# Kernel optimization log

Hardware: AMD Instinct MI355X
Metric: run time of the kernel (lower is better)

The kernel has to match this reference:

```python
import jax, jax.numpy as jnp
import numpy as np
from jax import lax

B, S, D, T = 64, 256, 1024, 60
HIST = 20  # last-20 window of attn / decoder-state history


def setup_inputs() -> dict:
    key = jax.random.key(0)
    ks = jax.random.split(key, 8)
    e_outputs = jax.random.normal(ks[0], (B, S, D), jnp.float32)
    queries = jax.random.normal(ks[1], (B, T, D), jnp.float32)
    # attention weights over source frames: rows sum to 1
    attns = jax.nn.softmax(jax.random.normal(ks[2], (B, T, S), jnp.float32), axis=-1)
    g = 0.02
    Wr = jax.random.normal(ks[3], (D, 1), jnp.float32) * g
    br = jnp.zeros((1,), jnp.float32)
    Wa = jax.random.normal(ks[4], (D, 1), jnp.float32) * g
    ba = jnp.zeros((1,), jnp.float32)
    Wq = jax.random.normal(ks[5], (D, D), jnp.float32) / np.sqrt(D)
    Wn = jax.random.normal(ks[6], (2 * D, 1), jnp.float32) * g
    bn = jnp.zeros((1,), jnp.float32)
    return {"e_outputs": e_outputs, "queries": queries, "attns": attns,
            "Wr": Wr, "br": br, "Wa": Wa, "ba": ba, "Wq": Wq, "Wn": Wn, "bn": bn}


def reference(e_outputs, queries, attns, Wr, br, Wa, ba, Wq, Wn, bn):
    Bn, Sn, Dn = e_outputs.shape
    # decay1[i] = (i+1)/20 ; decay2[i] = 1-(i+1)/50, zero-padded past 50 frames
    decay1 = (jnp.arange(HIST, dtype=jnp.float32) + 1.0) / 20.0
    idx = jnp.arange(Sn, dtype=jnp.float32)
    add0 = jnp.where(idx < 50, 1.0 - (idx + 1.0) / 50.0, 0.0)
    add_state0 = add0[None, :, None]                       # [1,S,1]
    mem0 = e_outputs * add_state0                          # [B,S,D]
    abuf0 = jnp.zeros((HIST, Bn, Sn), e_outputs.dtype)
    qbuf0 = jnp.zeros((HIST, Bn, Dn), e_outputs.dtype)

    def step(carry, x):
        mem, add_state, abuf, qbuf, i = carry
        attn_i, q_i = x                                    # [B,S], [B,D]
        # read: selected frame before memory update
        sel = jnp.einsum('bs,bsd->bd', attn_i, mem)
        # roll history buffers (newest at slot HIST-1)
        abuf = jnp.concatenate([abuf[1:], attn_i[None]], axis=0)
        qbuf = jnp.concatenate([qbuf[1:], q_i[None]], axis=0)
        k = jnp.minimum(i + 1, HIST)
        valid = jnp.arange(HIST) >= (HIST - k)
        temp = jax.nn.softmax(jnp.where(valid, decay1, -jnp.inf))
        attn_w = jnp.einsum('t,tbs->bs', temp, abuf)       # decayed attn sum
        query_s = jnp.einsum('t,tbd->bd', temp, qbuf)      # decayed query sum
        remove_prob = jax.nn.sigmoid(q_i @ Wr + br)[:, :, None]   # [B,1,1]
        add_prob = jax.nn.sigmoid(q_i @ Wa + ba)[:, :, None]      # [B,1,1]
        sim = jax.nn.sigmoid(jnp.einsum('bsd,bd->bs', mem, query_s @ Wq))[..., None]
        mem = mem * (1.0 - remove_prob * attn_w[..., None] * sim)
        last_ctx = jnp.einsum('bs,bsd->bd', attn_w, e_outputs)[:, None, :]
        cat = jnp.concatenate([e_outputs, jnp.broadcast_to(last_ctx, e_outputs.shape)], axis=-1)
        nxt = jax.nn.sigmoid(cat @ Wn + bn)                # [B,S,1]
        mem = mem + e_outputs * (1.0 - add_state) * (add_prob * nxt)
        add_state = add_state + (1.0 - add_state) * (add_prob * nxt)
        return (mem, add_state, abuf, qbuf, i + 1), sel

    init = (mem0, jnp.broadcast_to(add_state0, (Bn, Sn, 1)), abuf0, qbuf0, jnp.int32(0))
    xs = (attns.transpose(1, 0, 2), queries.transpose(1, 0, 2))
    _, sels = lax.scan(step, init, xs)
    return sels.transpose(1, 0, 2)                         # [B,T,D]
```

## Files before the change

### kernel.cpp

```cpp
#include <hip/hip_runtime.h>
#include <math.h>


#define Bn 64
#define Sn 256
#define Dn 1024
#define Tn 60
#define HISTn 20
#define LDK 72
#define K05 1.0512710963760241f
#define EINV 0.36787944117144233f

typedef __bf16 bf16x8 __attribute__((ext_vector_type(8)));
typedef float f32x4 __attribute__((ext_vector_type(4)));
typedef unsigned short us8 __attribute__((ext_vector_type(8)));

typedef const __attribute__((address_space(1))) unsigned int* gas_u32p;
typedef __attribute__((address_space(3))) unsigned int* las_u32p;

__device__ __forceinline__ void gl16(const unsigned short* g, unsigned short* l){
  __builtin_amdgcn_global_load_lds((gas_u32p)g, (las_u32p)l, 16, 0, 0);
}

__device__ __forceinline__ unsigned short f2bf(float f){
  unsigned int x; __builtin_memcpy(&x,&f,4);
  unsigned int lsb = (x >> 16) & 1u;
  x += 0x7fffu + lsb;
  return (unsigned short)(x >> 16);
}
__device__ __forceinline__ float sigmoidf_(float x){ return 1.0f/(1.0f+expf(-x)); }

__global__ __launch_bounds__(256) void conv_fused(
    const float* __restrict__ Q, const float* __restrict__ Wr,
    const float* __restrict__ br, const float* __restrict__ Wa,
    const float* __restrict__ ba, const float* __restrict__ Wq,
    const float* __restrict__ E, const float* __restrict__ Wn,
    float* __restrict__ rp, float* __restrict__ ap,
    unsigned short* __restrict__ Qbf, unsigned short* __restrict__ WT,
    unsigned short* __restrict__ Ebf,
    float* __restrict__ eW1, float* __restrict__ eW2)
{
  int tid = threadIdx.x;
  int bx = blockIdx.x;
  if (bx < Bn*Tn){
    int row = bx;
    float4 x = ((const float4*)(Q + (size_t)row*Dn))[tid];
    float4 a = ((const float4*)Wr)[tid];
    float4 b = ((const float4*)Wa)[tid];
    unsigned short o[4] = {f2bf(x.x), f2bf(x.y), f2bf(x.z), f2bf(x.w)};
    *(uint2*)&Qbf[(size_t)row*Dn + tid*4] = *(uint2*)o;
    float s1 = x.x*a.x + x.y*a.y + x.z*a.z + x.w*a.w;
    float s2 = x.x*b.x + x.y*b.y + x.z*b.z + x.w*b.w;
    for (int off = 32; off; off >>= 1){
      s1 += __shfl_down(s1, off, 64);
      s2 += __shfl_down(s2, off, 64);
    }
    __shared__ float r1[4], r2[4];
    int lane = tid & 63, wv = tid >> 6;
    if (lane == 0){ r1[wv] = s1; r2[wv] = s2; }
    __syncthreads();
    if (tid == 0){
      rp[row] = sigmoidf_(r1[0]+r1[1]+r1[2]+r1[3] + br[0]);
      ap[row] = sigmoidf_(r2[0]+r2[1]+r2[2]+r2[3] + ba[0]);
    }
  } else if (bx < Bn*Tn + 256){
    __shared__ __align__(16) unsigned short Tt[64][LDK];
    int t = bx - Bn*Tn;
    int n0 = (t >> 4)*64, k0 = (t & 15)*64;
    int kl = tid >> 4, nl4 = (tid & 15)*4;
    #pragma unroll
    for (int it = 0; it < 4; it++){
      int k = kl + it*16;
      float4 v = *(const float4*)&Wq[(size_t)(k0+k)*Dn + n0 + nl4];
      Tt[nl4+0][k] = f2bf(v.x); Tt[nl4+1][k] = f2bf(v.y);
      Tt[nl4+2][k] = f2bf(v.z); Tt[nl4+3][k] = f2bf(v.w);
    }
    __syncthreads();
    int nr = tid >> 2, kg = (tid & 3)*16;
    *(us8*)&WT[(size_t)(n0+nr)*Dn + k0+kg]   = *(us8*)&Tt[nr][kg];
    *(us8*)&WT[(size_t)(n0+nr)*Dn + k0+kg+8] = *(us8*)&Tt[nr][kg+8];
  } else {
    int row = (bx - (Bn*Tn + 256))*4 + (tid >> 6);
    int lane = tid & 63;
    const float* er = E + (size_t)row*Dn;
    unsigned short* ebr = Ebf + (size_t)row*Dn;
    float d1 = 0.f, d2 = 0.f;
    #pragma unroll
    for (int c = 0; c < 4; c++){
      int idx = c*64 + lane;
      float4 v = ((const float4*)er)[idx];
      float4 w1 = ((const float4*)Wn)[idx];
      float4 w2 = ((const float4*)(Wn + Dn))[idx];
      unsigned short o[4] = {f2bf(v.x), f2bf(v.y), f2bf(v.z), f2bf(v.w)};
      ((uint2*)ebr)[idx] = *(uint2*)o;
      d1 += v.x*w1.x + v.y*w1.y + v.z*w1.z + v.w*w1.w;
      d2 += v.x*w2.x + v.y*w2.y + v.z*w2.z + v.w*w2.w;
    }
    #pragma unroll
    for (int off = 32; off; off >>= 1){
      d1 += __shfl_down(d1, off, 64);
      d2 += __shfl_down(d2, off, 64);
    }
    if (lane == 0){ eW1[row] = d1; eW2[row] = d2; }
  }
}

__global__ __launch_bounds__(256) void gemm_qw_kr(
    const unsigned short* __restrict__ Qbf,
    const unsigned short* __restrict__ WT,
    const float* __restrict__ At,
    const float* __restrict__ eW2,
    unsigned short* __restrict__ QWbf,
    float* __restrict__ lc)
{
  int tid = threadIdx.x;
  if (blockIdx.x < (Bn*Tn/64)*(Dn/64)){
    __shared__ __align__(16) unsigned short As0_[64*64], Bs0_[64*64];
    __shared__ __align__(16) unsigned short As1_[64*64], Bs1_[64*64];
    int bx = (blockIdx.x & 7)*120 + (blockIdx.x >> 3);
    int m0 = (bx >> 4) * 64, n0 = (bx & 15) * 64;
    int lane = tid & 63, wave = tid >> 6;
    int quad = lane >> 4, l16 = lane & 15;
    f32x4 acc[4];
    #pragma unroll
    for (int nt=0;nt<4;nt++)
      #pragma unroll
      for (int r=0;r<4;r++) acc[nt][r]=0.f;
    int c0 = wave*2;
    int srow = c0*8 + (lane >> 3);
    int scol = ((lane & 7) ^ (lane >> 3)) * 8;
    const unsigned short* gA0 = Qbf + (size_t)(m0 + srow)*Dn + scol;
    const unsigned short* gA1 = gA0 + 8*Dn;
    const unsigned short* gB0 = WT  + (size_t)(n0 + srow)*Dn + scol;
    const unsigned short* gB1 = gB0 + 8*Dn;
    int mrow = wave*16 + l16;

    #define STAGE_QW(K, A_, B_) { \
      gl16(gA0 + (K), &A_[c0*512]);       \
      gl16(gA1 + (K), &A_[c0*512 + 512]); \
      gl16(gB0 + (K), &B_[c0*512]);       \
      gl16(gB1 + (K), &B_[c0*512 + 512]); }
    #define COMP_QW(A_, B_) { \
      _Pragma("unroll") \
      for (int kk = 0; kk < 2; kk++){ \
        bf16x8 a = *(const bf16x8*)&A_[ mrow*64 + ((kk*32 + quad*8) ^ ((mrow&7)*8)) ]; \
        _Pragma("unroll") \
        for (int nt=0;nt<4;nt++){ \
          int nrow = nt*16 + l16; \
          bf16x8 bb = *(const bf16x8*)&B_[ nrow*64 + ((kk*32 + quad*8) ^ ((nrow&7)*8)) ]; \
          acc[nt] = __builtin_amdgcn_mfma_f32_16x16x32_bf16(a, bb, acc[nt], 0, 0, 0); \
        } \
      } }

    STAGE_QW(0, As0_, Bs0_);
    __syncthreads();
    #pragma unroll
    for (int k0 = 0; k0 < Dn; k0 += 128){
      STAGE_QW(k0+64, As1_, Bs1_);
      COMP_QW(As0_, Bs0_);
      __syncthreads();
      if (k0+128 < Dn) STAGE_QW(k0+128, As0_, Bs0_);
      COMP_QW(As1_, Bs1_);
      __syncthreads();
    }
    #undef STAGE_QW
    #undef COMP_QW

    #pragma unroll
    for (int nt=0;nt<4;nt++)
      #pragma unroll
      for (int r=0;r<4;r++){
        int m = m0 + wave*16 + quad*4 + r;
        int n = n0 + nt*16 + l16;
        QWbf[(size_t)m*Dn + n] = f2bf(acc[nt][r]);
      }
  } else {
    int b = blockIdx.x - (Bn*Tn/64)*(Dn/64);
    int lane = tid & 63, wv = tid >> 6;
    __shared__ float Rsh[Tn];
    float4 e2v = ((const float4*)(eW2 + (size_t)b*Sn))[lane];
    const float* at_b = At + (size_t)b*Tn*Sn;
    #pragma unroll
    for (int w = 0; w < 15; w++){
      int j = wv + w*4;
      float4 a4 = ((const float4*)(at_b + (size_t)j*Sn))[lane];
      float v = a4.x*e2v.x + a4.y*e2v.y + a4.z*e2v.z + a4.w*e2v.w;
      #pragma unroll
      for (int off = 32; off; off >>= 1) v += __shfl_down(v, off, 64);
      if (lane == 0) Rsh[j] = v;
    }
    __syncthreads();
    if (tid < Tn){
      int i = tid;
      int j0 = (i - HISTn + 1 > 0) ? i - HISTn + 1 : 0;
      float num = 0.f, den = 0.f;
      float wj = 1.f;
      for (int j = 0; j <= i; j++){
        wj *= K05;
        if (j >= j0){ num += wj * Rsh[j]; den += wj; }
      }
      lc[b*Tn + i] = num / den;
    }
  }
}

__global__ __launch_bounds__(256) void g_scan(
    const unsigned short* __restrict__ QWbf,
    const unsigned short* __restrict__ Ebf,
    const float* __restrict__ At,
    const float* __restrict__ rp,
    const float* __restrict__ ap,
    const float* __restrict__ eW1,
    const float* __restrict__ lc,
    const float* __restrict__ bnp,
    unsigned short* __restrict__ Pbf)
{
  __shared__ __align__(16) unsigned short As0_[64][LDK], Bs0_[64][LDK];
  __shared__ __align__(16) unsigned short As1_[64][LDK], Bs1_[64][LDK];
  __shared__ __align__(16) float AtL[Tn][64], GL[Tn][64];
  __shared__ float lcs[Tn], rps[Tn], aps[Tn];
  int b = blockIdx.x, s0 = blockIdx.y * 64;
  int tid = threadIdx.x, lane = tid & 63, wave = tid >> 6;
  int quad = lane >> 4, l16 = lane & 15;

  const float* at_b = At + (size_t)b*Tn*Sn + s0;
  #pragma unroll
  for (int it = 0; it < 4; it++){
    int r = it*16 + (tid >> 4);
    if (r < Tn){
      int c4 = (tid & 15)*4;
      *(float4*)&AtL[r][c4] = *(const float4*)&at_b[(size_t)r*Sn + c4];
    }
  }
  if (tid < Tn){
    lcs[tid] = lc[b*Tn + tid];
    rps[tid] = rp[b*Tn + tid];
    aps[tid] = ap[b*Tn + tid];
  }

  f32x4 acc[4];
  #pragma unroll
  for (int nt=0;nt<4;nt++)
    #pragma unroll
    for (int r=0;r<4;r++) acc[nt][r]=0.f;
  int sr = tid >> 2, sk = (tid & 3)*16;
  const unsigned short* aRow = QWbf + ((size_t)(b*Tn + sr))*Dn;
  const unsigned short* bRow = Ebf  + ((size_t)(b*Sn + s0 + sr))*Dn;

  #define LOADR(K, ra0, ra1, rb0, rb1) { \
    if (sr < Tn){ ra0 = *(const us8*)&aRow[(K)+sk]; ra1 = *(const us8*)&aRow[(K)+sk+8]; } \
    else { ra0 = (us8)0; ra1 = (us8)0; } \
    rb0 = *(const us8*)&bRow[(K)+sk]; rb1 = *(const us8*)&bRow[(K)+sk+8]; }
  #define STORER(A_, B_, ra0, ra1, rb0, rb1) { \
    *(us8*)&A_[sr][sk]   = ra0; *(us8*)&A_[sr][sk+8] = ra1; \
    *(us8*)&B_[sr][sk]   = rb0; *(us8*)&B_[sr][sk+8] = rb1; }
  #define COMP_G(A_, B_) { \
    _Pragma("unroll") \
    for (int kk = 0; kk < 64; kk += 32){ \
      bf16x8 a = *(const bf16x8*)&A_[wave*16 + l16][kk + quad*8]; \
      _Pragma("unroll") \
      for (int nt=0;nt<4;nt++){ \
        bf16x8 bb = *(const bf16x8*)&B_[nt*16 + l16][kk + quad*8]; \
        acc[nt] = __builtin_amdgcn_mfma_f32_16x16x32_bf16(a, bb, acc[nt], 0, 0, 0); \
      } \
    } }

  us8 pa0, pa1, pb0, pb1, qa0, qa1, qb0, qb1;
  LOADR(0, pa0, pa1, pb0, pb1);
  STORER(As0_, Bs0_, pa0, pa1, pb0, pb1);
  for (int k0 = 0; k0 < Dn; k0 += 128){
    LOADR(k0+64, qa0, qa1, qb0, qb1);
    __syncthreads();
    COMP_G(As0_, Bs0_);
    STORER(As1_, Bs1_, qa0, qa1, qb0, qb1);
    if (k0+128 < Dn) LOADR(k0+128, pa0, pa1, pb0, pb1);
    __syncthreads();
    COMP_G(As1_, Bs1_);
    if (k0+128 < Dn) STORER(As0_, Bs0_, pa0, pa1, pb0, pb1);
  }
  #undef LOADR
  #undef STORER
  #undef COMP_G

  #pragma unroll
  for (int nt=0;nt<4;nt++)
    #pragma unroll
    for (int r=0;r<4;r++){
      int t = wave*16 + quad*4 + r;
      if (t < Tn) GL[t][nt*16 + l16] = acc[nt][r];
    }
  __syncthreads();

  if (tid < 64){
    int s = s0 + tid;
    float M = (s < 50) ? (1.0f - (s+1)/50.0f) : 0.0f;
    float A = M;
    float bnv = bnp[0];
    float e1 = eW1[b*Sn + s];
    unsigned short* P_b = Pbf + (size_t)b*Tn*Sn + s;
    float num_a = 0.f, num_q = 0.f, den = 0.f, wi = 1.f;
    #pragma unroll
    for (int i = 0; i < Tn; i++){
      wi *= K05;
      float a_new = AtL[i][tid];
      float g_new = GL[i][tid];
      num_a += wi * a_new;
      num_q += wi * g_new;
      den   += wi;
      if (i >= HISTn){
        float wo = wi * EINV;
        num_a -= wo * AtL[i-HISTn][tid];
        num_q -= wo * GL[i-HISTn][tid];
        den   -= wo;
      }
      float inv = 1.0f / den;
      float aw = num_a * inv;
      float qd = num_q * inv;
      P_b[(size_t)i*Sn] = f2bf(a_new * M);
      float sim = sigmoidf_(M * qd);
      float nxt = sigmoidf_(e1 + lcs[i] + bnv);
      M = M * (1.0f - rps[i] * aw * sim);
      float g = (1.0f - A) * aps[i] * nxt;
      M += g; A += g;
    }
  }
}

__global__ __launch_bounds__(256) void gemm_sels(
    const unsigned short* __restrict__ Pbf,
    const unsigned short* __restrict__ Ebf,
    float* __restrict__ out)
{
  __shared__ __align__(16) unsigned short As0_[64][LDK], Bs0_[64][LDK];
  __shared__ __align__(16) unsigned short As1_[64][LDK], Bs1_[64][LDK];
  int b = blockIdx.x, n0 = blockIdx.y*64;
  int tid = threadIdx.x, lane = tid & 63, wave = tid >> 6;
  int quad = lane >> 4, l16 = lane & 15;
  f32x4 acc[4];
  #pragma unroll
  for (int nt=0;nt<4;nt++)
    #pragma unroll
    for (int r=0;r<4;r++) acc[nt][r]=0.f;
  int sr = tid >> 2, sk = (tid & 3)*16;

  #define SLOAD(K, ra0, ra1, re0, re1) { \
    if (sr < Tn){ \
      const unsigned short* pp = &Pbf[((size_t)(b*Tn + sr))*Sn + (K)+sk]; \
      ra0 = *(const us8*)pp; ra1 = *(const us8*)(pp+8); \
    } else { ra0 = (us8)0; ra1 = (us8)0; } \
    const unsigned short* ep = &Ebf[((size_t)(b*Sn + (K) + sr))*Dn + n0 + sk]; \
    re0 = *(const us8*)ep; re1 = *(const us8*)(ep + 8); }
  #define SSTORE(A_, B_, ra0, ra1, re0, re1) { \
    *(us8*)&A_[sr][sk]   = ra0; *(us8*)&A_[sr][sk+8] = ra1; \
    _Pragma("unroll") \
    for (int j=0;j<8;j++){ \
      B_[sk+j][sr]   = re0[j]; \
      B_[sk+8+j][sr] = re1[j]; } }
  #define COMP_S(A_, B_) { \
    _Pragma("unroll") \
    for (int kk = 0; kk < 64; kk += 32){ \
      bf16x8 a = *(const bf16x8*)&A_[wave*16 + l16][kk + quad*8]; \
      _Pragma("unroll") \
      for (int nt=0;nt<4;nt++){ \
        bf16x8 bb = *(const bf16x8*)&B_[nt*16 + l16][kk + quad*8]; \
        acc[nt] = __builtin_amdgcn_mfma_f32_16x16x32_bf16(a, bb, acc[nt], 0, 0, 0); \
      } \
    } }

  us8 pa0, pa1, pe0, pe1, qa0, qa1, qe0, qe1;
  SLOAD(0, pa0, pa1, pe0, pe1);
  SSTORE(As0_, Bs0_, pa0, pa1, pe0, pe1);
  #pragma unroll
  for (int k0 = 0; k0 < Sn; k0 += 128){
    SLOAD(k0+64, qa0, qa1, qe0, qe1);
    __syncthreads();
    COMP_S(As0_, Bs0_);
    SSTORE(As1_, Bs1_, qa0, qa1, qe0, qe1);
    if (k0+128 < Sn) SLOAD(k0+128, pa0, pa1, pe0, pe1);
    __syncthreads();
    COMP_S(As1_, Bs1_);
    if (k0+128 < Sn) SSTORE(As0_, Bs0_, pa0, pa1, pe0, pe1);
  }
  #undef SLOAD
  #undef SSTORE
  #undef COMP_S

  #pragma unroll
  for (int nt=0;nt<4;nt++)
    #pragma unroll
    for (int r=0;r<4;r++){
      int t = wave*16 + quad*4 + r;
      int d = n0 + nt*16 + l16;
      if (t < Tn) out[((size_t)(b*Tn + t))*Dn + d] = acc[nt][r];
    }
}

extern "C" void kernel_launch(void* const* d_in, const int* in_sizes, int n_in,
                              void* d_out, int out_size, void* d_ws, size_t ws_size,
                              hipStream_t stream)
{
  const float* E  = (const float*)d_in[0];
  const float* Q  = (const float*)d_in[1];
  const float* At = (const float*)d_in[2];
  const float* Wr = (const float*)d_in[3];
  const float* br = (const float*)d_in[4];
  const float* Wa = (const float*)d_in[5];
  const float* ba = (const float*)d_in[6];
  const float* Wq = (const float*)d_in[7];
  const float* Wn = (const float*)d_in[8];
  const float* bnp= (const float*)d_in[9];

  char* ws = (char*)d_ws;
  float* rp  = (float*)ws; ws += (size_t)Bn*Tn*4;
  float* ap  = (float*)ws; ws += (size_t)Bn*Tn*4;
  float* eW1 = (float*)ws; ws += (size_t)Bn*Sn*4;
  float* eW2 = (float*)ws; ws += (size_t)Bn*Sn*4;
  float* lcb = (float*)ws; ws += (size_t)Bn*Tn*4;
  unsigned short* Qbf  = (unsigned short*)ws; ws += (size_t)Bn*Tn*Dn*2;
  unsigned short* WT   = (unsigned short*)ws; ws += (size_t)Dn*Dn*2;
  unsigned short* QWbf = (unsigned short*)ws; ws += (size_t)Bn*Tn*Dn*2;
  unsigned short* Ebf  = (unsigned short*)ws; ws += (size_t)Bn*Sn*Dn*2;
  unsigned short* Pbf = (unsigned short*)ws; ws += (size_t)Bn*Tn*Sn*2;

  conv_fused<<<Bn*Tn + 256 + Bn*Sn/4, 256, 0, stream>>>(
      Q, Wr, br, Wa, ba, Wq, E, Wn, rp, ap, Qbf, WT, Ebf, eW1, eW2);
  gemm_qw_kr<<<(Bn*Tn/64)*(Dn/64) + Bn, 256, 0, stream>>>(
      Qbf, WT, At, eW2, QWbf, lcb);
  g_scan<<<dim3(Bn, Sn/64), 256, 0, stream>>>(
      QWbf, Ebf, At, rp, ap, eW1, lcb, bnp, Pbf);
  gemm_sels<<<dim3(Bn, Dn/64), 256, 0, stream>>>(Pbf, Ebf, (float*)d_out);
}
```

Baseline: 184.1 us.

## Rebalance kernel stages: move E conversion into QW GEMM, fuse lc into scan

The E fp32-to-bf16 conversion and Wn dot products move from the first kernel into the QW GEMM launch as extra blocks. The per-batch lc computation (attn·eW2 plus a decayed window sum) moves into g_scan, where each block recomputes it redundantly. g_scan now uses 32-column S tiles, which doubles its grid, and gemm_sels drops from a double-buffered LDS pipeline to a single buffer. The aim is to even out work across launches and give the scan stage more parallelism, at the cost of redundant lc work per block and less load/compute overlap in gemm_sels.

```diff
diff --git a/kernel.cpp b/kernel.cpp
--- a/kernel.cpp
+++ b/kernel.cpp
@@ -30,15 +30,12 @@
 }
 __device__ __forceinline__ float sigmoidf_(float x){ return 1.0f/(1.0f+expf(-x)); }
 
-__global__ __launch_bounds__(256) void conv_fused(
+__global__ __launch_bounds__(256) void convQW(
     const float* __restrict__ Q, const float* __restrict__ Wr,
     const float* __restrict__ br, const float* __restrict__ Wa,
     const float* __restrict__ ba, const float* __restrict__ Wq,
-    const float* __restrict__ E, const float* __restrict__ Wn,
     float* __restrict__ rp, float* __restrict__ ap,
-    unsigned short* __restrict__ Qbf, unsigned short* __restrict__ WT,
-    unsigned short* __restrict__ Ebf,
-    float* __restrict__ eW1, float* __restrict__ eW2)
+    unsigned short* __restrict__ Qbf, unsigned short* __restrict__ WT)
 {
   int tid = threadIdx.x;
   int bx = blockIdx.x;
@@ -63,7 +60,7 @@
       rp[row] = sigmoidf_(r1[0]+r1[1]+r1[2]+r1[3] + br[0]);
       ap[row] = sigmoidf_(r2[0]+r2[1]+r2[2]+r2[3] + ba[0]);
     }
-  } else if (bx < Bn*Tn + 256){
+  } else {
     __shared__ __align__(16) unsigned short Tt[64][LDK];
     int t = bx - Bn*Tn;
     int n0 = (t >> 4)*64, k0 = (t & 15)*64;
@@ -79,39 +76,16 @@
     int nr = tid >> 2, kg = (tid & 3)*16;
     *(us8*)&WT[(size_t)(n0+nr)*Dn + k0+kg]   = *(us8*)&Tt[nr][kg];
     *(us8*)&WT[(size_t)(n0+nr)*Dn + k0+kg+8] = *(us8*)&Tt[nr][kg+8];
-  } else {
-    int row = (bx - (Bn*Tn + 256))*4 + (tid >> 6);
-    int lane = tid & 63;
-    const float* er = E + (size_t)row*Dn;
-    unsigned short* ebr = Ebf + (size_t)row*Dn;
-    float d1 = 0.f, d2 = 0.f;
-    #pragma unroll
-    for (int c = 0; c < 4; c++){
-      int idx = c*64 + lane;
-      float4 v = ((const float4*)er)[idx];
-      float4 w1 = ((const float4*)Wn)[idx];
-      float4 w2 = ((const float4*)(Wn + Dn))[idx];
-      unsigned short o[4] = {f2bf(v.x), f2bf(v.y), f2bf(v.z), f2bf(v.w)};
-      ((uint2*)ebr)[idx] = *(uint2*)o;
-      d1 += v.x*w1.x + v.y*w1.y + v.z*w1.z + v.w*w1.w;
-      d2 += v.x*w2.x + v.y*w2.y + v.z*w2.z + v.w*w2.w;
-    }
-    #pragma unroll
-    for (int off = 32; off; off >>= 1){
-      d1 += __shfl_down(d1, off, 64);
-      d2 += __shfl_down(d2, off, 64);
-    }
-    if (lane == 0){ eW1[row] = d1; eW2[row] = d2; }
-  }
-}
-
-__global__ __launch_bounds__(256) void gemm_qw_kr(
+  }
+}
+
+__global__ __launch_bounds__(256) void qw_e(
     const unsigned short* __restrict__ Qbf,
     const unsigned short* __restrict__ WT,
-    const float* __restrict__ At,
-    const float* __restrict__ eW2,
+    const float* __restrict__ E, const float* __restrict__ Wn,
     unsigned short* __restrict__ QWbf,
-    float* __restrict__ lc)
+    unsigned short* __restrict__ Ebf,
+    float* __restrict__ eW1, float* __restrict__ eW2)
 {
   int tid = threadIdx.x;
   if (blockIdx.x < (Bn*Tn/64)*(Dn/64)){
@@ -175,32 +149,28 @@
         QWbf[(size_t)m*Dn + n] = f2bf(acc[nt][r]);
       }
   } else {
-    int b = blockIdx.x - (Bn*Tn/64)*(Dn/64);
-    int lane = tid & 63, wv = tid >> 6;
-    __shared__ float Rsh[Tn];
-    float4 e2v = ((const float4*)(eW2 + (size_t)b*Sn))[lane];
-    const float* at_b = At + (size_t)b*Tn*Sn;
-    #pragma unroll
-    for (int w = 0; w < 15; w++){
-      int j = wv + w*4;
-      float4 a4 = ((const float4*)(at_b + (size_t)j*Sn))[lane];
-      float v = a4.x*e2v.x + a4.y*e2v.y + a4.z*e2v.z + a4.w*e2v.w;
-      #pragma unroll
-      for (int off = 32; off; off >>= 1) v += __shfl_down(v, off, 64);
-      if (lane == 0) Rsh[j] = v;
-    }
-    __syncthreads();
-    if (tid < Tn){
-      int i = tid;
-      int j0 = (i - HISTn + 1 > 0) ? i - HISTn + 1 : 0;
-      float num = 0.f, den = 0.f;
-      float wj = 1.f;
-      for (int j = 0; j <= i; j++){
-        wj *= K05;
-        if (j >= j0){ num += wj * Rsh[j]; den += wj; }
-      }
-      lc[b*Tn + i] = num / den;
-    }
+    int row = (blockIdx.x - (Bn*Tn/64)*(Dn/64))*4 + (tid >> 6);
+    int lane = tid & 63;
+    const float* er = E + (size_t)row*Dn;
+    unsigned short* ebr = Ebf + (size_t)row*Dn;
+    float d1 = 0.f, d2 = 0.f;
+    #pragma unroll
+    for (int c = 0; c < 4; c++){
+      int idx = c*64 + lane;
+      float4 v = ((const float4*)er)[idx];
+      float4 w1 = ((const float4*)Wn)[idx];
+      float4 w2 = ((const float4*)(Wn + Dn))[idx];
+      unsigned short o[4] = {f2bf(v.x), f2bf(v.y), f2bf(v.z), f2bf(v.w)};
+      ((uint2*)ebr)[idx] = *(uint2*)o;
+      d1 += v.x*w1.x + v.y*w1.y + v.z*w1.z + v.w*w1.w;
+      d2 += v.x*w2.x + v.y*w2.y + v.z*w2.z + v.w*w2.w;
+    }
+    #pragma unroll
+    for (int off = 32; off; off >>= 1){
+      d1 += __shfl_down(d1, off, 64);
+      d2 += __shfl_down(d2, off, 64);
+    }
+    if (lane == 0){ eW1[row] = d1; eW2[row] = d2; }
   }
 }
 
@@ -211,79 +181,92 @@
     const float* __restrict__ rp,
     const float* __restrict__ ap,
     const float* __restrict__ eW1,
-    const float* __restrict__ lc,
+    const float* __restrict__ eW2,
     const float* __restrict__ bnp,
     unsigned short* __restrict__ Pbf)
 {
-  __shared__ __align__(16) unsigned short As0_[64][LDK], Bs0_[64][LDK];
-  __shared__ __align__(16) unsigned short As1_[64][LDK], Bs1_[64][LDK];
-  __shared__ __align__(16) float AtL[Tn][64], GL[Tn][64];
-  __shared__ float lcs[Tn], rps[Tn], aps[Tn];
-  int b = blockIdx.x, s0 = blockIdx.y * 64;
+  __shared__ __align__(16) unsigned short As0_[64][LDK], As1_[64][LDK];
+  __shared__ __align__(16) unsigned short Bs0_[32][LDK], Bs1_[32][LDK];
+  __shared__ __align__(16) float AtL[Tn][32], GL[Tn][32];
+  __shared__ float Rsh[Tn], lcs[Tn], rps[Tn], aps[Tn];
+  int b = blockIdx.x, s0 = blockIdx.y * 32;
   int tid = threadIdx.x, lane = tid & 63, wave = tid >> 6;
   int quad = lane >> 4, l16 = lane & 15;
 
-  const float* at_b = At + (size_t)b*Tn*Sn + s0;
-  #pragma unroll
-  for (int it = 0; it < 4; it++){
-    int r = it*16 + (tid >> 4);
-    if (r < Tn){
-      int c4 = (tid & 15)*4;
-      *(float4*)&AtL[r][c4] = *(const float4*)&at_b[(size_t)r*Sn + c4];
+  {
+    float4 e2v = ((const float4*)(eW2 + (size_t)b*Sn))[lane];
+    const float* at_b = At + (size_t)b*Tn*Sn;
+    #pragma unroll
+    for (int w = 0; w < 15; w++){
+      int j = wave + w*4;
+      float4 a4 = ((const float4*)(at_b + (size_t)j*Sn))[lane];
+      float v = a4.x*e2v.x + a4.y*e2v.y + a4.z*e2v.z + a4.w*e2v.w;
+      #pragma unroll
+      for (int off = 32; off; off >>= 1) v += __shfl_down(v, off, 64);
+      if (lane == 0) Rsh[j] = v;
+    }
+  }
+  {
+    const float* at_c = At + (size_t)b*Tn*Sn + s0;
+    #pragma unroll
+    for (int it = 0; it < 2; it++){
+      int idx = it*256 + tid;
+      int r = idx >> 3, c4 = (idx & 7)*4;
+      if (r < Tn) *(float4*)&AtL[r][c4] = *(const float4*)&at_c[(size_t)r*Sn + c4];
     }
   }
   if (tid < Tn){
-    lcs[tid] = lc[b*Tn + tid];
     rps[tid] = rp[b*Tn + tid];
     aps[tid] = ap[b*Tn + tid];
   }
 
-  f32x4 acc[4];
+  f32x4 acc[2];
   #pragma unroll
-  for (int nt=0;nt<4;nt++)
+  for (int nt=0;nt<2;nt++)
     #pragma unroll
     for (int r=0;r<4;r++) acc[nt][r]=0.f;
   int sr = tid >> 2, sk = (tid & 3)*16;
+  int brw = tid >> 3, bk = (tid & 7)*8;
   const unsigned short* aRow = QWbf + ((size_t)(b*Tn + sr))*Dn;
-  const unsigned short* bRow = Ebf  + ((size_t)(b*Sn + s0 + sr))*Dn;
-
-  #define LOADR(K, ra0, ra1, rb0, rb1) { \
+  const unsigned short* bRow = Ebf  + ((size_t)(b*Sn + s0 + brw))*Dn;
+
+  #define LOADR(K, ra0, ra1, rb0) { \
     if (sr < Tn){ ra0 = *(const us8*)&aRow[(K)+sk]; ra1 = *(const us8*)&aRow[(K)+sk+8]; } \
     else { ra0 = (us8)0; ra1 = (us8)0; } \
-    rb0 = *(const us8*)&bRow[(K)+sk]; rb1 = *(const us8*)&bRow[(K)+sk+8]; }
-  #define STORER(A_, B_, ra0, ra1, rb0, rb1) { \
+    rb0 = *(const us8*)&bRow[(K)+bk]; }
+  #define STORER(A_, B_, ra0, ra1, rb0) { \
     *(us8*)&A_[sr][sk]   = ra0; *(us8*)&A_[sr][sk+8] = ra1; \
-    *(us8*)&B_[sr][sk]   = rb0; *(us8*)&B_[sr][sk+8] = rb1; }
+    *(us8*)&B_[brw][bk]  = rb0; }
   #define COMP_G(A_, B_) { \
     _Pragma("unroll") \
     for (int kk = 0; kk < 64; kk += 32){ \
       bf16x8 a = *(const bf16x8*)&A_[wave*16 + l16][kk + quad*8]; \
       _Pragma("unroll") \
-      for (int nt=0;nt<4;nt++){ \
+      for (int nt=0;nt<2;nt++){ \
         bf16x8 bb = *(const bf16x8*)&B_[nt*16 + l16][kk + quad*8]; \
         acc[nt] = __builtin_amdgcn_mfma_f32_16x16x32_bf16(a, bb, acc[nt], 0, 0, 0); \
       } \
     } }
 
-  us8 pa0, pa1, pb0, pb1, qa0, qa1, qb0, qb1;
-  LOADR(0, pa0, pa1, pb0, pb1);
-  STORER(As0_, Bs0_, pa0, pa1, pb0, pb1);
+  us8 pa0, pa1, pb0, qa0, qa1, qb0;
+  LOADR(0, pa0, pa1, pb0);
+  STORER(As0_, Bs0_, pa0, pa1, pb0);
   for (int k0 = 0; k0 < Dn; k0 += 128){
-    LOADR(k0+64, qa0, qa1, qb0, qb1);
+    LOADR(k0+64, qa0, qa1, qb0);
     __syncthreads();
     COMP_G(As0_, Bs0_);
-    STORER(As1_, Bs1_, qa0, qa1, qb0, qb1);
-    if (k0+128 < Dn) LOADR(k0+128, pa0, pa1, pb0, pb1);
+    STORER(As1_, Bs1_, qa0, qa1, qb0);
+    if (k0+128 < Dn) LOADR(k0+128, pa0, pa1, pb0);
     __syncthreads();
     COMP_G(As1_, Bs1_);
-    if (k0+128 < Dn) STORER(As0_, Bs0_, pa0, pa1, pb0, pb1);
+    if (k0+128 < Dn) STORER(As0_, Bs0_, pa0, pa1, pb0);
   }
   #undef LOADR
   #undef STORER
   #undef COMP_G
 
   #pragma unroll
-  for (int nt=0;nt<4;nt++)
+  for (int nt=0;nt<2;nt++)
     #pragma unroll
     for (int r=0;r<4;r++){
       int t = wave*16 + quad*4 + r;
@@ -291,7 +274,19 @@
     }
   __syncthreads();
 
-  if (tid < 64){
+  if (tid < Tn){
+    int i = tid;
+    int j0 = (i - HISTn + 1 > 0) ? i - HISTn + 1 : 0;
+    float num = 0.f, den = 0.f, wj = 1.f;
+    for (int j = 0; j <= i; j++){
+      wj *= K05;
+      if (j >= j0){ num += wj * Rsh[j]; den += wj; }
+    }
+    lcs[i] = num / den;
+  }
+  __syncthreads();
+
+  if (tid < 32){
     int s = s0 + tid;
     float M = (s < 50) ? (1.0f - (s+1)/50.0f) : 0.0f;
     float A = M;
@@ -331,8 +326,7 @@
     const unsigned short* __restrict__ Ebf,
     float* __restrict__ out)
 {
-  __shared__ __align__(16) unsigned short As0_[64][LDK], Bs0_[64][LDK];
-  __shared__ __align__(16) unsigned short As1_[64][LDK], Bs1_[64][LDK];
+  __shared__ __align__(16) unsigned short As_[64][LDK], Bs_[64][LDK];
   int b = blockIdx.x, n0 = blockIdx.y*64;
   int tid = threadIdx.x, lane = tid & 63, wave = tid >> 6;
   int quad = lane >> 4, l16 = lane & 15;
@@ -343,43 +337,40 @@
     for (int r=0;r<4;r++) acc[nt][r]=0.f;
   int sr = tid >> 2, sk = (tid & 3)*16;
 
-  #define SLOAD(K, ra0, ra1, re0, re1) { \
+  #define SLOAD(K) { \
     if (sr < Tn){ \
       const unsigned short* pp = &Pbf[((size_t)(b*Tn + sr))*Sn + (K)+sk]; \
-      ra0 = *(const us8*)pp; ra1 = *(const us8*)(pp+8); \
-    } else { ra0 = (us8)0; ra1 = (us8)0; } \
+      pa0 = *(const us8*)pp; pa1 = *(const us8*)(pp+8); \
+    } else { pa0 = (us8)0; pa1 = (us8)0; } \
     const unsigned short* ep = &Ebf[((size_t)(b*Sn + (K) + sr))*Dn + n0 + sk]; \
-    re0 = *(const us8*)ep; re1 = *(const us8*)(ep + 8); }
-  #define SSTORE(A_, B_, ra0, ra1, re0, re1) { \
-    *(us8*)&A_[sr][sk]   = ra0; *(us8*)&A_[sr][sk+8] = ra1; \
+    pe0 = *(const us8*)ep; pe1 = *(const us8*)(ep + 8); }
+  #define SSTORE() { \
+    *(us8*)&As_[sr][sk]   = pa0; *(us8*)&As_[sr][sk+8] = pa1; \
     _Pragma("unroll") \
     for (int j=0;j<8;j++){ \
-      B_[sk+j][sr]   = re0[j]; \
-      B_[sk+8+j][sr] = re1[j]; } }
-  #define COMP_S(A_, B_) { \
+      Bs_[sk+j][sr]   = pe0[j]; \
+      Bs_[sk+8+j][sr] = pe1[j]; } }
+  #define COMP_S() { \
     _Pragma("unroll") \
     for (int kk = 0; kk < 64; kk += 32){ \
-      bf16x8 a = *(const bf16x8*)&A_[wave*16 + l16][kk + quad*8]; \
+      bf16x8 a = *(const bf16x8*)&As_[wave*16 + l16][kk + quad*8]; \
       _Pragma("unroll") \
       for (int nt=0;nt<4;nt++){ \
-        bf16x8 bb = *(const bf16x8*)&B_[nt*16 + l16][kk + quad*8]; \
+        bf16x8 bb = *(const bf16x8*)&Bs_[nt*16 + l16][kk + quad*8]; \
         acc[nt] = __builtin_amdgcn_mfma_f32_16x16x32_bf16(a, bb, acc[nt], 0, 0, 0); \
       } \
     } }
 
-  us8 pa0, pa1, pe0, pe1, qa0, qa1, qe0, qe1;
-  SLOAD(0, pa0, pa1, pe0, pe1);
-  SSTORE(As0_, Bs0_, pa0, pa1, pe0, pe1);
+  us8 pa0, pa1, pe0, pe1;
+  SLOAD(0);
+  SSTORE();
   #pragma unroll
-  for (int k0 = 0; k0 < Sn; k0 += 128){
-    SLOAD(k0+64, qa0, qa1, qe0, qe1);
-    __syncthreads();
-    COMP_S(As0_, Bs0_);
-    SSTORE(As1_, Bs1_, qa0, qa1, qe0, qe1);
-    if (k0+128 < Sn) SLOAD(k0+128, pa0, pa1, pe0, pe1);
-    __syncthreads();
-    COMP_S(As1_, Bs1_);
-    if (k0+128 < Sn) SSTORE(As0_, Bs0_, pa0, pa1, pe0, pe1);
+  for (int k0 = 0; k0 < Sn; k0 += 64){
+    __syncthreads();
+    if (k0+64 < Sn) SLOAD(k0+64);
+    COMP_S();
+    __syncthreads();
+    if (k0+64 < Sn) SSTORE();
   }
   #undef SLOAD
   #undef SSTORE
@@ -415,18 +406,17 @@
   float* ap  = (float*)ws; ws += (size_t)Bn*Tn*4;
   float* eW1 = (float*)ws; ws += (size_t)Bn*Sn*4;
   float* eW2 = (float*)ws; ws += (size_t)Bn*Sn*4;
-  float* lcb = (float*)ws; ws += (size_t)Bn*Tn*4;
   unsigned short* Qbf  = (unsigned short*)ws; ws += (size_t)Bn*Tn*Dn*2;
   unsigned short* WT   = (unsigned short*)ws; ws += (size_t)Dn*Dn*2;
   unsigned short* QWbf = (unsigned short*)ws; ws += (size_t)Bn*Tn*Dn*2;
   unsigned short* Ebf  = (unsigned short*)ws; ws += (size_t)Bn*Sn*Dn*2;
   unsigned short* Pbf = (unsigned short*)ws; ws += (size_t)Bn*Tn*Sn*2;
 
-  conv_fused<<<Bn*Tn + 256 + Bn*Sn/4, 256, 0, stream>>>(
-      Q, Wr, br, Wa, ba, Wq, E, Wn, rp, ap, Qbf, WT, Ebf, eW1, eW2);
-  gemm_qw_kr<<<(Bn*Tn/64)*(Dn/64) + Bn, 256, 0, stream>>>(
-      Qbf, WT, At, eW2, QWbf, lcb);
-  g_scan<<<dim3(Bn, Sn/64), 256, 0, stream>>>(
-      QWbf, Ebf, At, rp, ap, eW1, lcb, bnp, Pbf);
+  convQW<<<Bn*Tn + 256, 256, 0, stream>>>(
+      Q, Wr, br, Wa, ba, Wq, rp, ap, Qbf, WT);
+  qw_e<<<(Bn*Tn/64)*(Dn/64) + Bn*Sn/4, 256, 0, stream>>>(
+      Qbf, WT, E, Wn, QWbf, Ebf, eW1, eW2);
+  g_scan<<<dim3(Bn, Sn/32), 256, 0, stream>>>(
+      QWbf, Ebf, At, rp, ap, eW1, eW2, bnp, Pbf);
   gemm_sels<<<dim3(Bn, Dn/64), 256, 0, stream>>>(Pbf, Ebf, (float*)d_out);
 }
```

Result: slower. 189.9 us (+3.2%).
